# Kernel tuning notes

Measured on AMD Instinct MI355X. Metric: run time of the kernel, lower is better.

The kernel has to match this reference:

```python
import jax, jax.numpy as jnp
import numpy as np

T_TEST, B, F, H, N_OUT = 8192, 8, 100, 512, 1


def setup_inputs() -> dict:
    key = jax.random.key(0)
    ks = jax.random.split(key, 7)
    s = 0.05  # keep generated-weight magnitudes in a realistic hypernetwork range
    return {
        "x_test": jax.random.normal(ks[0], (T_TEST, B, F), dtype=jnp.float32),
        "w1": jax.random.normal(ks[1], (B, F, H), dtype=jnp.float32) * s,
        "b1": jax.random.normal(ks[2], (B, H), dtype=jnp.float32) * s,
        "w2": jax.random.normal(ks[3], (B, H, H), dtype=jnp.float32) * s,
        "b2": jax.random.normal(ks[4], (B, H), dtype=jnp.float32) * s,
        "w3": jax.random.normal(ks[5], (B, H, N_OUT), dtype=jnp.float32) * s,
        "b3": jax.random.normal(ks[6], (B, N_OUT), dtype=jnp.float32) * s,
    }


def reference(x_test, w1, b1, w2, b2, w3, b3):
    # MotherNet.nn_forward with predicted_activation='relu',
    # weight_embedding_rank=None, low_rank_last=False.
    # Original torch: h = (x.unsqueeze(-1) * w.unsqueeze(0)).sum(2) + b
    # == per-dataset batched GEMM over the B axis.
    x = jnp.nan_to_num(x_test)                    # [T, B, F]
    h = jnp.einsum('tbf,bfh->tbh', x, w1) + b1    # [T, B, H]
    h = jax.nn.relu(h)
    h = jnp.einsum('tbf,bfh->tbh', h, w2) + b2    # [T, B, H]
    h = jax.nn.relu(h)
    h = jnp.einsum('tbf,bfh->tbh', h, w3) + b3    # [T, B, 1]
    return h
```

## Files before the change

### kernel.cpp

```cpp
#include <hip/hip_runtime.h>

#define T_TEST 8192
#define BB 8
#define FF 100
#define HH 512

typedef __bf16 bf16x8 __attribute__((ext_vector_type(8)));
typedef float f32x16 __attribute__((ext_vector_type(16)));
typedef unsigned short u16;
typedef unsigned int u32;

__device__ __forceinline__ u16 f2bf(float f) {
    u32 u = __float_as_uint(f);
    u += 0x7fffu + ((u >> 16) & 1);
    return (u16)(u >> 16);
}

__device__ __forceinline__ float nan2num(float v) {
    u32 u = __float_as_uint(v);
    if ((u & 0x7f800000u) == 0x7f800000u) {
        v = (u & 0x007fffffu) ? 0.f : ((u >> 31) ? -3.3895314e38f : 3.3895314e38f);
    }
    return v;
}

__global__ void prep_w(const float* __restrict__ w1, const float* __restrict__ w2,
                       u16* __restrict__ w1f, u16* __restrict__ w2f) {
    int bid = blockIdx.x;
    if (bid < 256) {
        int t = bid * 256 + threadIdx.x;
        int lane = t & 63;
        int n32 = (t >> 6) & 15;
        int b = t >> 13;
        int n = n32 * 32 + (lane & 31);
        int kb = ((t >> 10) & 7) * 16 + (lane >> 5) * 8;
        u32 p[4];
#pragma unroll
        for (int jp = 0; jp < 4; ++jp) {
            int k0 = kb + jp * 2;
            float v0 = (k0 < FF)     ? w1[(b * FF + k0) * HH + n]     : 0.f;
            float v1 = (k0 + 1 < FF) ? w1[(b * FF + k0 + 1) * HH + n] : 0.f;
            p[jp] = (u32)f2bf(v0) | ((u32)f2bf(v1) << 16);
        }
        uint4 o = {p[0], p[1], p[2], p[3]};
        *(uint4*)(w1f + (size_t)t * 8) = o;
    } else {
        int t = (bid - 256) * 256 + threadIdx.x;
        int lane = t & 63;
        int n32 = (t >> 6) & 15;
        int b = t >> 15;
        int n = n32 * 32 + (lane & 31);
        int kb = ((t >> 10) & 31) * 16 + (lane >> 5) * 8;
        u32 p[4];
#pragma unroll
        for (int jp = 0; jp < 4; ++jp) {
            int k0 = kb + jp * 2;
            float v0 = w2[(b * HH + k0) * HH + n];
            float v1 = w2[(b * HH + k0 + 1) * HH + n];
            p[jp] = (u32)f2bf(v0) | ((u32)f2bf(v1) << 16);
        }
        uint4 o = {p[0], p[1], p[2], p[3]};
        *(uint4*)(w2f + (size_t)t * 8) = o;
    }
}

__global__ __launch_bounds__(512, 4) void fused_mlp(
    const float* __restrict__ x, const u16* __restrict__ w1f,
    const float* __restrict__ b1, const u16* __restrict__ w2f,
    const float* __restrict__ b2, const float* __restrict__ w3,
    const float* __restrict__ b3, float* __restrict__ out) {
    __shared__ __align__(16) char lds[81920];
    u16* xf  = (u16*)lds;
    u16* h1f = (u16*)(lds + 16384);

    const int tid = threadIdx.x;
    const int b = blockIdx.x;
    const int m0 = blockIdx.y * 64;
    const int lane = tid & 63;
    const int ws = __builtin_amdgcn_readfirstlane(tid >> 6);
    const int l31 = lane & 31, lh = lane >> 5;
    const int n32b = ws * 2;
    const int r2 = ws * 4;

    const bf16x8* W1 = (const bf16x8*)w1f + (size_t)b * 8192;
    const bf16x8* W2 = (const bf16x8*)w2f + (size_t)b * 32768;

    bf16x8 pa[3][2], pb[3][2];

#pragma unroll
    for (int s = 0; s < 2; ++s)
#pragma unroll
        for (int ni = 0; ni < 2; ++ni)
            pb[s][ni] = W1[(s * 16 + n32b + ni) * 64 + lane];

    {
        int row = tid >> 3, sub = tid & 7;
        int mi = row >> 5, m = row & 31;
        const float* xr = x + ((size_t)(m0 + row) * BB + b) * FF + sub * 16;
        u32 p[8];
#pragma unroll
        for (int i = 0; i < 8; ++i) p[i] = 0;
        if (sub <= 5) {
#pragma unroll
            for (int j = 0; j < 4; ++j) {
                float4 v = *(const float4*)(xr + j * 4);
                p[j * 2 + 0] = (u32)f2bf(nan2num(v.x)) | ((u32)f2bf(nan2num(v.y)) << 16);
                p[j * 2 + 1] = (u32)f2bf(nan2num(v.z)) | ((u32)f2bf(nan2num(v.w)) << 16);
            }
        } else if (sub == 6) {
            float4 v = *(const float4*)(xr);
            p[0] = (u32)f2bf(nan2num(v.x)) | ((u32)f2bf(nan2num(v.y)) << 16);
            p[1] = (u32)f2bf(nan2num(v.z)) | ((u32)f2bf(nan2num(v.w)) << 16);
        }
        int fi1 = sub * 2 + mi;
        uint4 g0 = {p[0], p[1], p[2], p[3]};
        uint4 g1 = {p[4], p[5], p[6], p[7]};
        *(uint4*)(xf + (fi1 * 64 + m) * 8)      = g0;
        *(uint4*)(xf + (fi1 * 64 + 32 + m) * 8) = g1;
    }
    __syncthreads();

    f32x16 acc1[2][2] = {};
#pragma unroll
    for (int s = 0; s < 2; ++s)
#pragma unroll
        for (int mi = 0; mi < 2; ++mi)
            pa[s][mi] = *(const bf16x8*)(xf + ((s * 2 + mi) * 64 + lane) * 8);
#pragma unroll
    for (int ks = 0; ks < 8; ++ks) {
        const int p = ks % 3;
        if (ks < 6) {
            const int f = (ks + 2) % 3;
#pragma unroll
            for (int mi = 0; mi < 2; ++mi)
                pa[f][mi] = *(const bf16x8*)(xf + (((ks + 2) * 2 + mi) * 64 + lane) * 8);
#pragma unroll
            for (int ni = 0; ni < 2; ++ni)
                pb[f][ni] = W1[((ks + 2) * 16 + n32b + ni) * 64 + lane];
        }
#pragma unroll
        for (int ni = 0; ni < 2; ++ni) {
            acc1[0][ni] = __builtin_amdgcn_mfma_f32_32x32x16_bf16(pa[p][0], pb[p][ni], acc1[0][ni], 0, 0, 0);
            acc1[1][ni] = __builtin_amdgcn_mfma_f32_32x32x16_bf16(pa[p][1], pb[p][ni], acc1[1][ni], 0, 0, 0);
        }
    }

#pragma unroll
    for (int s = 0; s < 2; ++s)
#pragma unroll
        for (int ni = 0; ni < 2; ++ni)
            pb[s][ni] = W2[((r2 + s) * 16 + n32b + ni) * 64 + lane];

    {
        const float* b1g = b1 + b * HH;
        char* hw = (char*)h1f + (l31 >> 4) * 2048 + ((l31 >> 3) & 1) * 512 +
                   (l31 & 6) * 2 + lh * 64 + n32b * 4096;
#pragma unroll
        for (int ni = 0; ni < 2; ++ni) {
            float b1v = b1g[(n32b + ni) * 32 + l31];
#pragma unroll
            for (int mi = 0; mi < 2; ++mi)
#pragma unroll
                for (int qd = 0; qd < 4; ++qd) {
                    u32 own01 = (u32)f2bf(fmaxf(acc1[mi][ni][qd * 4 + 0] + b1v, 0.f)) |
                                ((u32)f2bf(fmaxf(acc1[mi][ni][qd * 4 + 1] + b1v, 0.f)) << 16);
                    u32 own23 = (u32)f2bf(fmaxf(acc1[mi][ni][qd * 4 + 2] + b1v, 0.f)) |
                                ((u32)f2bf(fmaxf(acc1[mi][ni][qd * 4 + 3] + b1v, 0.f)) << 16);
                    u32 oth01 = __shfl_xor(own01, 1, 64);
                    u32 oth23 = __shfl_xor(own23, 1, 64);
                    char* base = hw + ni * 4096 + mi * 1024 + qd * 128;
                    if (!(lane & 1)) {
                        *(u32*)(base +  0) = (own01 & 0xffffu) | (oth01 << 16);
                        *(u32*)(base + 16) = (own01 >> 16) | (oth01 & 0xffff0000u);
                    } else {
                        *(u32*)(base + 32) = (oth23 & 0xffffu) | (own23 << 16);
                        *(u32*)(base + 48) = (oth23 >> 16) | (own23 & 0xffff0000u);
                    }
                }
        }
    }
    __syncthreads();

    f32x16 acc2[2][2] = {};
    const char* hv  = (const char*)h1f + r2 * 2048 + (size_t)lane * 16;
    const char* hvB = hv - 65536;
#pragma unroll
    for (int s = 0; s < 2; ++s)
#pragma unroll
        for (int mi = 0; mi < 2; ++mi)
            pa[s][mi] = *(const bf16x8*)(hv + s * 2048 + mi * 1024);
#pragma unroll
    for (int ks = 0; ks < 32; ++ks) {
        const int p = ks % 3;
        if (ks < 30) {
            const int f = (ks + 2) % 3;
            const char* hp = (ks + 2 + r2 < 32) ? hv : hvB;
#pragma unroll
            for (int mi = 0; mi < 2; ++mi)
                pa[f][mi] = *(const bf16x8*)(hp + (ks + 2) * 2048 + mi * 1024);
            int kspf = ks + 2 + r2;
            kspf -= (kspf >= 32) ? 32 : 0;
#pragma unroll
            for (int ni = 0; ni < 2; ++ni)
                pb[f][ni] = W2[(kspf * 16 + n32b + ni) * 64 + lane];
        }
#pragma unroll
        for (int ni = 0; ni < 2; ++ni) {
            acc2[0][ni] = __builtin_amdgcn_mfma_f32_32x32x16_bf16(pa[p][0], pb[p][ni], acc2[0][ni], 0, 0, 0);
            acc2[1][ni] = __builtin_amdgcn_mfma_f32_32x32x16_bf16(pa[p][1], pb[p][ni], acc2[1][ni], 0, 0, 0);
        }
    }

    const float* b2g = b2 + b * HH;
    const float* w3g = w3 + b * HH;
    float b2v[2], w3v[2];
#pragma unroll
    for (int ni = 0; ni < 2; ++ni) {
        int n = (n32b + ni) * 32 + l31;
        b2v[ni] = b2g[n];
        w3v[ni] = w3g[n];
    }
    float* part = (float*)xf;
#pragma unroll
    for (int mi = 0; mi < 2; ++mi)
#pragma unroll
        for (int r = 0; r < 16; ++r) {
            float v = fmaxf(acc2[mi][0][r] + b2v[0], 0.f) * w3v[0] +
                      fmaxf(acc2[mi][1][r] + b2v[1], 0.f) * w3v[1];
            v += __shfl_xor(v, 1, 64);
            v += __shfl_xor(v, 2, 64);
            v += __shfl_xor(v, 4, 64);
            v += __shfl_xor(v, 8, 64);
            v += __shfl_xor(v, 16, 64);
            if (l31 == 0)
                part[ws * 64 + mi * 32 + (r & 3) + 8 * (r >> 2) + 4 * lh] = v;
        }
    __syncthreads();
    if (tid < 64) {
        float s = b3[b];
#pragma unroll
        for (int ww = 0; ww < 8; ++ww) s += part[ww * 64 + tid];
        out[(size_t)(m0 + tid) * BB + b] = s;
    }
}

extern "C" void kernel_launch(void* const* d_in, const int* in_sizes, int n_in,
                              void* d_out, int out_size, void* d_ws, size_t ws_size,
                              hipStream_t stream) {
    const float* x  = (const float*)d_in[0];
    const float* w1 = (const float*)d_in[1];
    const float* b1 = (const float*)d_in[2];
    const float* w2 = (const float*)d_in[3];
    const float* b2 = (const float*)d_in[4];
    const float* w3 = (const float*)d_in[5];
    const float* b3 = (const float*)d_in[6];
    float* out = (float*)d_out;

    u16* w1f = (u16*)d_ws;
    u16* w2f = w1f + (size_t)BB * 8192 * 8;

    prep_w<<<1280, 256, 0, stream>>>(w1, w2, w1f, w2f);

    fused_mlp<<<dim3(BB, T_TEST / 64), 512, 0, stream>>>(
        x, w1f, b1, w2f, b2, w3, b3, out);
}
```

Measured before the change: 141.8 us.

## Deepen global weight prefetch to four stages and swap grid axis order

The MFMA loops now keep LDS activation fragments double-buffered but prefetch global weight fragments four k-steps ahead instead of two. This aims to hide more global-load latency. The grid is transposed so consecutive blocks share the same dataset b, which may improve L2 reuse of that dataset's weights. The x-staging mapping is changed so each wave handles one feature chunk for 64 rows, and the b2/w3 loads are hoisted ahead of the second GEMM. Holding more prefetched fragments raises register pressure under launch_bounds(512,4).

After: 138.2 us. -2.5%, faster.

```diff
diff --git a/kernel.cpp b/kernel.cpp
--- a/kernel.cpp
+++ b/kernel.cpp
@@ -74,8 +74,8 @@
     u16* h1f = (u16*)(lds + 16384);
 
     const int tid = threadIdx.x;
-    const int b = blockIdx.x;
-    const int m0 = blockIdx.y * 64;
+    const int b = blockIdx.y;
+    const int m0 = blockIdx.x * 64;
     const int lane = tid & 63;
     const int ws = __builtin_amdgcn_readfirstlane(tid >> 6);
     const int l31 = lane & 31, lh = lane >> 5;
@@ -85,34 +85,34 @@
     const bf16x8* W1 = (const bf16x8*)w1f + (size_t)b * 8192;
     const bf16x8* W2 = (const bf16x8*)w2f + (size_t)b * 32768;
 
-    bf16x8 pa[3][2], pb[3][2];
-
-#pragma unroll
-    for (int s = 0; s < 2; ++s)
+    bf16x8 pa[2][2], pb[4][2];
+
+#pragma unroll
+    for (int s = 0; s < 4; ++s)
 #pragma unroll
         for (int ni = 0; ni < 2; ++ni)
             pb[s][ni] = W1[(s * 16 + n32b + ni) * 64 + lane];
 
     {
-        int row = tid >> 3, sub = tid & 7;
+        int row = lane, s = ws;
         int mi = row >> 5, m = row & 31;
-        const float* xr = x + ((size_t)(m0 + row) * BB + b) * FF + sub * 16;
+        const float* xr = x + ((size_t)(m0 + row) * BB + b) * FF + s * 16;
         u32 p[8];
 #pragma unroll
         for (int i = 0; i < 8; ++i) p[i] = 0;
-        if (sub <= 5) {
+        if (s <= 5) {
 #pragma unroll
             for (int j = 0; j < 4; ++j) {
                 float4 v = *(const float4*)(xr + j * 4);
                 p[j * 2 + 0] = (u32)f2bf(nan2num(v.x)) | ((u32)f2bf(nan2num(v.y)) << 16);
                 p[j * 2 + 1] = (u32)f2bf(nan2num(v.z)) | ((u32)f2bf(nan2num(v.w)) << 16);
             }
-        } else if (sub == 6) {
+        } else if (s == 6) {
             float4 v = *(const float4*)(xr);
             p[0] = (u32)f2bf(nan2num(v.x)) | ((u32)f2bf(nan2num(v.y)) << 16);
             p[1] = (u32)f2bf(nan2num(v.z)) | ((u32)f2bf(nan2num(v.w)) << 16);
         }
-        int fi1 = sub * 2 + mi;
+        int fi1 = s * 2 + mi;
         uint4 g0 = {p[0], p[1], p[2], p[3]};
         uint4 g1 = {p[4], p[5], p[6], p[7]};
         *(uint4*)(xf + (fi1 * 64 + m) * 8)      = g0;
@@ -128,28 +128,32 @@
             pa[s][mi] = *(const bf16x8*)(xf + ((s * 2 + mi) * 64 + lane) * 8);
 #pragma unroll
     for (int ks = 0; ks < 8; ++ks) {
-        const int p = ks % 3;
+        const int pA = ks & 1, pB = ks & 3;
+        bf16x8 a0 = pa[pA][0], a1 = pa[pA][1];
+        bf16x8 b0 = pb[pB][0], b1r = pb[pB][1];
         if (ks < 6) {
-            const int f = (ks + 2) % 3;
 #pragma unroll
             for (int mi = 0; mi < 2; ++mi)
-                pa[f][mi] = *(const bf16x8*)(xf + (((ks + 2) * 2 + mi) * 64 + lane) * 8);
+                pa[pA][mi] = *(const bf16x8*)(xf + (((ks + 2) * 2 + mi) * 64 + lane) * 8);
+        }
+        if (ks < 4) {
 #pragma unroll
             for (int ni = 0; ni < 2; ++ni)
-                pb[f][ni] = W1[((ks + 2) * 16 + n32b + ni) * 64 + lane];
-        }
-#pragma unroll
-        for (int ni = 0; ni < 2; ++ni) {
-            acc1[0][ni] = __builtin_amdgcn_mfma_f32_32x32x16_bf16(pa[p][0], pb[p][ni], acc1[0][ni], 0, 0, 0);
-            acc1[1][ni] = __builtin_amdgcn_mfma_f32_32x32x16_bf16(pa[p][1], pb[p][ni], acc1[1][ni], 0, 0, 0);
-        }
-    }
-
-#pragma unroll
-    for (int s = 0; s < 2; ++s)
+                pb[pB][ni] = W1[((ks + 4) * 16 + n32b + ni) * 64 + lane];
+        }
+        acc1[0][0] = __builtin_amdgcn_mfma_f32_32x32x16_bf16(a0, b0,  acc1[0][0], 0, 0, 0);
+        acc1[0][1] = __builtin_amdgcn_mfma_f32_32x32x16_bf16(a0, b1r, acc1[0][1], 0, 0, 0);
+        acc1[1][0] = __builtin_amdgcn_mfma_f32_32x32x16_bf16(a1, b0,  acc1[1][0], 0, 0, 0);
+        acc1[1][1] = __builtin_amdgcn_mfma_f32_32x32x16_bf16(a1, b1r, acc1[1][1], 0, 0, 0);
+    }
+
+#pragma unroll
+    for (int s = 0; s < 4; ++s) {
+        int k = (r2 + s) & 31;
 #pragma unroll
         for (int ni = 0; ni < 2; ++ni)
-            pb[s][ni] = W2[((r2 + s) * 16 + n32b + ni) * 64 + lane];
+            pb[s][ni] = W2[(k * 16 + n32b + ni) * 64 + lane];
+    }
 
     {
         const float* b1g = b1 + b * HH;
@@ -181,45 +185,52 @@
     }
     __syncthreads();
 
+    float b2v[2], w3v[2];
+    {
+        const float* b2g = b2 + b * HH;
+        const float* w3g = w3 + b * HH;
+#pragma unroll
+        for (int ni = 0; ni < 2; ++ni) {
+            int n = (n32b + ni) * 32 + l31;
+            b2v[ni] = b2g[n];
+            w3v[ni] = w3g[n];
+        }
+    }
+
     f32x16 acc2[2][2] = {};
     const char* hv  = (const char*)h1f + r2 * 2048 + (size_t)lane * 16;
     const char* hvB = hv - 65536;
 #pragma unroll
-    for (int s = 0; s < 2; ++s)
+    for (int s = 0; s < 2; ++s) {
+        const char* hp = (s + r2 < 32) ? hv : hvB;
 #pragma unroll
         for (int mi = 0; mi < 2; ++mi)
-            pa[s][mi] = *(const bf16x8*)(hv + s * 2048 + mi * 1024);
+            pa[s][mi] = *(const bf16x8*)(hp + s * 2048 + mi * 1024);
+    }
 #pragma unroll
     for (int ks = 0; ks < 32; ++ks) {
-        const int p = ks % 3;
+        const int pA = ks & 1, pB = ks & 3;
+        bf16x8 a0 = pa[pA][0], a1 = pa[pA][1];
+        bf16x8 b0 = pb[pB][0], b1r = pb[pB][1];
         if (ks < 30) {
-            const int f = (ks + 2) % 3;
             const char* hp = (ks + 2 + r2 < 32) ? hv : hvB;
 #pragma unroll
             for (int mi = 0; mi < 2; ++mi)
-                pa[f][mi] = *(const bf16x8*)(hp + (ks + 2) * 2048 + mi * 1024);
-            int kspf = ks + 2 + r2;
+                pa[pA][mi] = *(const bf16x8*)(hp + (ks + 2) * 2048 + mi * 1024);
+        }
+        if (ks < 28) {
+            int kspf = ks + 4 + r2;
             kspf -= (kspf >= 32) ? 32 : 0;
 #pragma unroll
             for (int ni = 0; ni < 2; ++ni)
-                pb[f][ni] = W2[(kspf * 16 + n32b + ni) * 64 + lane];
-        }
-#pragma unroll
-        for (int ni = 0; ni < 2; ++ni) {
-            acc2[0][ni] = __builtin_amdgcn_mfma_f32_32x32x16_bf16(pa[p][0], pb[p][ni], acc2[0][ni], 0, 0, 0);
-            acc2[1][ni] = __builtin_amdgcn_mfma_f32_32x32x16_bf16(pa[p][1], pb[p][ni], acc2[1][ni], 0, 0, 0);
-        }
-    }
-
-    const float* b2g = b2 + b * HH;
-    const float* w3g = w3 + b * HH;
-    float b2v[2], w3v[2];
-#pragma unroll
-    for (int ni = 0; ni < 2; ++ni) {
-        int n = (n32b + ni) * 32 + l31;
-        b2v[ni] = b2g[n];
-        w3v[ni] = w3g[n];
-    }
+                pb[pB][ni] = W2[(kspf * 16 + n32b + ni) * 64 + lane];
+        }
+        acc2[0][0] = __builtin_amdgcn_mfma_f32_32x32x16_bf16(a0, b0,  acc2[0][0], 0, 0, 0);
+        acc2[0][1] = __builtin_amdgcn_mfma_f32_32x32x16_bf16(a0, b1r, acc2[0][1], 0, 0, 0);
+        acc2[1][0] = __builtin_amdgcn_mfma_f32_32x32x16_bf16(a1, b0,  acc2[1][0], 0, 0, 0);
+        acc2[1][1] = __builtin_amdgcn_mfma_f32_32x32x16_bf16(a1, b1r, acc2[1][1], 0, 0, 0);
+    }
+
     float* part = (float*)xf;
 #pragma unroll
     for (int mi = 0; mi < 2; ++mi)
@@ -261,6 +272,6 @@
 
     prep_w<<<1280, 256, 0, stream>>>(w1, w2, w1f, w2f);
 
-    fused_mlp<<<dim3(BB, T_TEST / 64), 512, 0, stream>>>(
+    fused_mlp<<<dim3(T_TEST / 64, BB), 512, 0, stream>>>(
         x, w1f, b1, w2f, b2, w3, b3, out);
 }
```
